# Optimization experiments

Hardware: AMD Instinct MI355X
Metric: run time of the kernel (lower is better)

The kernel has to match this reference:

```python
import jax, jax.numpy as jnp
import numpy as np

N_NODES = 100000
N_EDGES = 1600000
D_IN = 128
D_HID = 128
N_CLASS = 10
N_GRAPHS = 512
BN_EPS = 1e-5


def setup_inputs() -> dict:
    key = jax.random.key(0)
    ks = jax.random.split(key, 12)
    x = jax.random.normal(ks[0], (N_NODES, D_IN), dtype=jnp.float32)
    edge_index = jax.random.randint(ks[1], (2, N_EDGES), 0, N_NODES, dtype=jnp.int32)
    idx = jnp.sort(jax.random.randint(ks[2], (N_NODES,), 0, N_GRAPHS, dtype=jnp.int32))
    s = 1.0 / np.sqrt(D_HID)
    W1 = jax.random.uniform(ks[3], (D_IN, D_HID), minval=-s, maxval=s, dtype=jnp.float32)
    b1 = jnp.zeros((D_HID,), jnp.float32)
    W2 = jax.random.uniform(ks[4], (D_HID, D_HID), minval=-s, maxval=s, dtype=jnp.float32)
    b2 = jnp.zeros((D_HID,), jnp.float32)
    W3 = jax.random.uniform(ks[5], (D_HID, D_HID), minval=-s, maxval=s, dtype=jnp.float32)
    b3 = jnp.zeros((D_HID,), jnp.float32)
    W4 = jax.random.uniform(ks[6], (D_HID, N_CLASS), minval=-s, maxval=s, dtype=jnp.float32)
    b4 = jnp.zeros((N_CLASS,), jnp.float32)
    gamma = jnp.ones((D_HID,), jnp.float32)
    beta = jnp.zeros((D_HID,), jnp.float32)
    return {"x": x, "edge_index": edge_index, "idx": idx,
            "W1": W1, "b1": b1, "W2": W2, "b2": b2,
            "W3": W3, "b3": b3, "W4": W4, "b4": b4,
            "gamma": gamma, "beta": beta}


def _agg(h, src, dst):
    # (adj + I) @ h : sum of neighbor features plus self-loop
    return jax.ops.segment_sum(h[src], dst, num_segments=N_NODES) + h


def reference(x, edge_index, idx, W1, b1, W2, b2, W3, b3, W4, b4, gamma, beta):
    src, dst = edge_index[0], edge_index[1]
    z1 = jax.nn.relu(_agg(x, src, dst) @ W1 + b1)          # [N, H] (dropout = identity, eval)
    h = _agg(z1, src, dst) @ W2 + b2                        # [N, H]
    pooled = jax.ops.segment_sum(h, idx, num_segments=N_GRAPHS)  # [G, H] scatter-add readout
    # BatchNorm1d over graph (batch) dimension, training-mode batch stats
    mean = jnp.mean(pooled, axis=0)
    var = jnp.var(pooled, axis=0)
    out = (pooled - mean) * jax.lax.rsqrt(var + BN_EPS) * gamma + beta
    zg = jax.nn.relu(out @ W3 + b3)
    logits = zg @ W4 + b4                                   # [G, C]
    return jax.nn.log_softmax(logits, axis=1)
```

## Files before the change

kernel.cpp:

```cpp
#include <hip/hip_runtime.h>
#include <hip/hip_fp16.h>
#include <math.h>

#define NN 100000
#define NE 1600000
#define DH 128
#define NG 512
#define NC 10
#define NSEG 8
#define SEGN 12500
#define CHE 8192
#define NCH 196
#define MAXDEG 48

#define NB_HIST (NCH * NSEG)
#define NB_CNT  98
#define NB_GEMM ((NN + 63) / 64)


typedef __attribute__((ext_vector_type(8))) _Float16 f16x8;
typedef __attribute__((ext_vector_type(4))) float f32x4;
typedef __attribute__((ext_vector_type(4))) int i32x4;


__device__ __forceinline__ void upd_edge(int d, int s, int lo, int hi,
                                         int* __restrict__ counts,
                                         int* __restrict__ csr) {
    if (d >= lo && d < hi) {
        int p = atomicAdd(&counts[d], 1);
        if (p < MAXDEG) csr[d * MAXDEG + p] = s;
    }
}

__global__ __launch_bounds__(256, 8) void k_hist(
    const int* __restrict__ dst, const int* __restrict__ src,
    int* __restrict__ counts, int* __restrict__ csr,
    const int* __restrict__ gidx, int* __restrict__ cnt) {
    int b = blockIdx.x;
    int t = threadIdx.x;
    if (b < NB_HIST) {
        int seg = b & 7;
        int chunk = b >> 3;
        int lo = seg * SEGN, hi = lo + SEGN;
        int e0 = chunk * CHE;
        int e1 = e0 + CHE < NE ? e0 + CHE : NE;
        for (int e = e0 + t * 8; e < e1; e += 2048) {
            i32x4 da = __builtin_nontemporal_load((const i32x4*)(dst + e));
            i32x4 db = __builtin_nontemporal_load((const i32x4*)(dst + e + 4));
            i32x4 sa = __builtin_nontemporal_load((const i32x4*)(src + e));
            i32x4 sb = __builtin_nontemporal_load((const i32x4*)(src + e + 4));
            upd_edge(da.x, sa.x, lo, hi, counts, csr);
            upd_edge(da.y, sa.y, lo, hi, counts, csr);
            upd_edge(da.z, sa.z, lo, hi, counts, csr);
            upd_edge(da.w, sa.w, lo, hi, counts, csr);
            upd_edge(db.x, sb.x, lo, hi, counts, csr);
            upd_edge(db.y, sb.y, lo, hi, counts, csr);
            upd_edge(db.z, sb.z, lo, hi, counts, csr);
            upd_edge(db.w, sb.w, lo, hi, counts, csr);
        }
    } else {
        int cb = b - NB_HIST;
        int n0 = cb * 1024 + t * 4;
        if (n0 >= NN) return;
        int g = gidx[n0];
        int run = 1;
        for (int j = 1; j < 4; ++j) {
            int n = n0 + j;
            if (n < NN) {
                int gg = gidx[n];
                if (gg == g) {
                    run++;
                } else {
                    atomicAdd(&cnt[g], run);
                    g = gg;
                    run = 1;
                }
            }
        }
        atomicAdd(&cnt[g], run);
    }
}


__global__ __launch_bounds__(256, 4) void k_gemm(
    const float* __restrict__ A, const float* __restrict__ W,
    __half* __restrict__ out) {
    __shared__ _Float16 sWT[DH * 128];
    int gb = blockIdx.x;
    int t = threadIdx.x;
    int wv = t >> 6;
    int lane = t & 63;
    for (int i = t; i < DH * DH; i += 256) {
        int k = i >> 7, n = i & 127;
        sWT[n * 128 + (((k >> 3) ^ (n & 15)) * 8) + (k & 7)] = (_Float16)W[i];
    }
    __syncthreads();

    int m = lane & 15;
    int quad = lane >> 4;
    int node0 = gb * 64 + wv * 16;
    int nodeA = node0 + m;
    if (nodeA >= NN) nodeA = NN - 1;
    const float* arow = A + (size_t)nodeA * DH;

    f16x8 afrag[4];
#pragma unroll
    for (int kt = 0; kt < 4; ++kt) {
        int k0 = kt * 32 + quad * 8;
        f32x4 u0 = __builtin_nontemporal_load((const f32x4*)(arow + k0));
        f32x4 u1 = __builtin_nontemporal_load((const f32x4*)(arow + k0 + 4));
        afrag[kt][0] = (_Float16)u0.x; afrag[kt][1] = (_Float16)u0.y;
        afrag[kt][2] = (_Float16)u0.z; afrag[kt][3] = (_Float16)u0.w;
        afrag[kt][4] = (_Float16)u1.x; afrag[kt][5] = (_Float16)u1.y;
        afrag[kt][6] = (_Float16)u1.z; afrag[kt][7] = (_Float16)u1.w;
    }

    f32x4 acc0 = {0.f, 0.f, 0.f, 0.f};
    f32x4 acc1 = acc0, acc2 = acc0, acc3 = acc0;
    f32x4 acc4 = acc0, acc5 = acc0, acc6 = acc0, acc7 = acc0;
#pragma unroll
    for (int kt = 0; kt < 4; ++kt) {
        int kb = kt * 4 + quad;
        const _Float16* wbase = &sWT[(size_t)m * 128 + ((kb ^ m) * 8)];
        acc0 = __builtin_amdgcn_mfma_f32_16x16x32_f16(afrag[kt], *(const f16x8*)(wbase + 0 * 16 * 128), acc0, 0, 0, 0);
        acc1 = __builtin_amdgcn_mfma_f32_16x16x32_f16(afrag[kt], *(const f16x8*)(wbase + 1 * 16 * 128), acc1, 0, 0, 0);
        acc2 = __builtin_amdgcn_mfma_f32_16x16x32_f16(afrag[kt], *(const f16x8*)(wbase + 2 * 16 * 128), acc2, 0, 0, 0);
        acc3 = __builtin_amdgcn_mfma_f32_16x16x32_f16(afrag[kt], *(const f16x8*)(wbase + 3 * 16 * 128), acc3, 0, 0, 0);
        acc4 = __builtin_amdgcn_mfma_f32_16x16x32_f16(afrag[kt], *(const f16x8*)(wbase + 4 * 16 * 128), acc4, 0, 0, 0);
        acc5 = __builtin_amdgcn_mfma_f32_16x16x32_f16(afrag[kt], *(const f16x8*)(wbase + 5 * 16 * 128), acc5, 0, 0, 0);
        acc6 = __builtin_amdgcn_mfma_f32_16x16x32_f16(afrag[kt], *(const f16x8*)(wbase + 6 * 16 * 128), acc6, 0, 0, 0);
        acc7 = __builtin_amdgcn_mfma_f32_16x16x32_f16(afrag[kt], *(const f16x8*)(wbase + 7 * 16 * 128), acc7, 0, 0, 0);
    }

#pragma unroll
    for (int r = 0; r < 4; ++r) {
        int node = node0 + quad * 4 + r;
        if (node < NN) {
            uint4 o;
            *(__half2*)&o.x = __floats2half2_rn(acc0[r], acc1[r]);
            *(__half2*)&o.y = __floats2half2_rn(acc2[r], acc3[r]);
            *(__half2*)&o.z = __floats2half2_rn(acc4[r], acc5[r]);
            *(__half2*)&o.w = __floats2half2_rn(acc6[r], acc7[r]);
            ((uint4*)out)[(size_t)node * 16 + m] = o;
        }
    }
}


__device__ __forceinline__ void acc8(float* a, const uint4& v, float m) {
    float2 f;
    f = __half22float2(*(const __half2*)&v.x); a[0] = fmaf(m, f.x, a[0]); a[1] = fmaf(m, f.y, a[1]);
    f = __half22float2(*(const __half2*)&v.y); a[2] = fmaf(m, f.x, a[2]); a[3] = fmaf(m, f.y, a[3]);
    f = __half22float2(*(const __half2*)&v.z); a[4] = fmaf(m, f.x, a[4]); a[5] = fmaf(m, f.y, a[5]);
    f = __half22float2(*(const __half2*)&v.w); a[6] = fmaf(m, f.x, a[6]); a[7] = fmaf(m, f.y, a[7]);
}


__global__ __launch_bounds__(256, 4) void k_agg_h(
    const __half* __restrict__ in, const int* __restrict__ counts,
    const int* __restrict__ csr, const float* __restrict__ bias,
    __half* __restrict__ outA) {
    int t = threadIdx.x;
    int lane = t & 15;
    int node = blockIdx.x * 16 + (t >> 4);
    const uint4* in4 = (const uint4*)in;
    float a[8];
#pragma unroll
    for (int j = 0; j < 8; ++j) a[j] = 0.f;
    uint4 sv = in4[(size_t)node * 16 + lane];
    acc8(a, sv, 1.f);
    int e0 = node * MAXDEG;
    int deg = counts[node];
    deg = deg < MAXDEG ? deg : MAXDEG;
    int e1 = e0 + deg;
    int elast = e1 - 1;
    for (int e = e0; e < e1; e += 8) {
        int idx[8];
        float m[8];
#pragma unroll
        for (int i = 0; i < 8; ++i) {
            int ei = e + i;
            int ec = ei < elast ? ei : elast;
            idx[i] = csr[ec];
            m[i] = (ei < e1) ? 1.f : 0.f;
        }
        uint4 v[8];
#pragma unroll
        for (int i = 0; i < 8; ++i) v[i] = in4[(size_t)idx[i] * 16 + lane];
#pragma unroll
        for (int i = 0; i < 8; ++i) acc8(a, v[i], m[i]);
    }
    float bj[8];
#pragma unroll
    for (int j = 0; j < 8; ++j) bj[j] = bias[j * 16 + lane];
#pragma unroll
    for (int j = 0; j < 8; ++j) a[j] = fmaxf(a[j] + bj[j], 0.f);
    uint4 o;
    *(__half2*)&o.x = __floats2half2_rn(a[0], a[1]);
    *(__half2*)&o.y = __floats2half2_rn(a[2], a[3]);
    *(__half2*)&o.z = __floats2half2_rn(a[4], a[5]);
    *(__half2*)&o.w = __floats2half2_rn(a[6], a[7]);
    ((uint4*)outA)[(size_t)node * 16 + lane] = o;
}


__global__ __launch_bounds__(256, 4) void k_agg_pool_h(
    const __half* __restrict__ in, const int* __restrict__ counts,
    const int* __restrict__ csr, const int* __restrict__ gidx,
    float* __restrict__ pp8) {
    __shared__ __align__(16) float sA[16][DH];
    int t = threadIdx.x;
    int lane = t & 15;
    int p = t >> 4;
    int node0 = blockIdx.x * 16;
    int node = node0 + p;
    const uint4* in4 = (const uint4*)in;
    float a[8];
#pragma unroll
    for (int j = 0; j < 8; ++j) a[j] = 0.f;
    uint4 sv = in4[(size_t)node * 16 + lane];
    acc8(a, sv, 1.f);
    int e0 = node * MAXDEG;
    int deg = counts[node];
    deg = deg < MAXDEG ? deg : MAXDEG;
    int e1 = e0 + deg;
    int elast = e1 - 1;
    for (int e = e0; e < e1; e += 8) {
        int idx[8];
        float m[8];
#pragma unroll
        for (int i = 0; i < 8; ++i) {
            int ei = e + i;
            int ec = ei < elast ? ei : elast;
            idx[i] = csr[ec];
            m[i] = (ei < e1) ? 1.f : 0.f;
        }
        uint4 v[8];
#pragma unroll
        for (int i = 0; i < 8; ++i) v[i] = in4[(size_t)idx[i] * 16 + lane];
#pragma unroll
        for (int i = 0; i < 8; ++i) acc8(a, v[i], m[i]);
    }
    float4* row = (float4*)&sA[p][lane * 8];
    row[0] = make_float4(a[0], a[1], a[2], a[3]);
    row[1] = make_float4(a[4], a[5], a[6], a[7]);
    __syncthreads();
    if (t < DH) {
        float* pp = pp8 + (size_t)(blockIdx.x & 7) * NG * DH;
        int gprev = gidx[node0];
        float run = 0.f;
        for (int q = 0; q < 16; ++q) {
            int g = gidx[node0 + q];
            if (g != gprev) {
                atomicAdd(&pp[gprev * DH + t], run);
                run = 0.f;
                gprev = g;
            }
            run += sA[q][t];
        }
        atomicAdd(&pp[gprev * DH + t], run);
    }
}


__device__ __forceinline__ void fma4(float4& acc, float s, const float4& wv) {
    acc.x = fmaf(s, wv.x, acc.x);
    acc.y = fmaf(s, wv.y, acc.y);
    acc.z = fmaf(s, wv.z, acc.z);
    acc.w = fmaf(s, wv.w, acc.w);
}


__global__ __launch_bounds__(256, 2) void k_pool_mm(
    const float* __restrict__ pp8, const float* __restrict__ W,
    const float* __restrict__ bias, const int* __restrict__ cnt,
    float* __restrict__ pooled) {
    __shared__ __align__(16) float sW[DH * DH];
    __shared__ __align__(16) float sA[32 * DH];
    int t = threadIdx.x;
    int g0 = blockIdx.x * 32;
    {
        const float4* W4g = (const float4*)W;
        float4* sW4 = (float4*)sW;
        for (int i = t; i < DH * DH / 4; i += 256) {
            int r = i >> 5;
            int orig = ((r & 7) << 4) + (r >> 3);
            sW4[i] = W4g[orig * 32 + (i & 31)];
        }
        const float4* P4 = (const float4*)pp8;
        float4* sA4 = (float4*)sA;
        for (int i = t; i < 32 * DH / 4; i += 256) {
            float4 s;
            s.x = 0.f; s.y = 0.f; s.z = 0.f; s.w = 0.f;
#pragma unroll
            for (int c = 0; c < NSEG; ++c) {
                float4 v = P4[(size_t)c * NG * DH / 4 + (size_t)g0 * DH / 4 + i];
                s.x += v.x; s.y += v.y; s.z += v.z; s.w += v.w;
            }
            sA4[i] = s;
        }
    }
    __syncthreads();

    int c4 = t & 31;
    int n0 = (t >> 5) * 4;
    const float4* sA4 = (const float4*)sA;
    const float4* sW4 = (const float4*)sW;
    float4 acc0, acc1, acc2, acc3;
    acc0.x = acc0.y = acc0.z = acc0.w = 0.f;
    acc1 = acc0; acc2 = acc0; acc3 = acc0;

#pragma unroll 2
    for (int kc = 0; kc < DH / 4; ++kc) {
        float4 a0 = sA4[(n0 + 0) * 32 + kc];
        float4 a1 = sA4[(n0 + 1) * 32 + kc];
        float4 a2 = sA4[(n0 + 2) * 32 + kc];
        float4 a3 = sA4[(n0 + 3) * 32 + kc];
        float4 w0 = sW4[(4 * kc + 0) * 32 + c4];
        float4 w1 = sW4[(4 * kc + 1) * 32 + c4];
        float4 w2 = sW4[(4 * kc + 2) * 32 + c4];
        float4 w3 = sW4[(4 * kc + 3) * 32 + c4];
        fma4(acc0, a0.x, w0); fma4(acc0, a0.y, w1); fma4(acc0, a0.z, w2); fma4(acc0, a0.w, w3);
        fma4(acc1, a1.x, w0); fma4(acc1, a1.y, w1); fma4(acc1, a1.z, w2); fma4(acc1, a1.w, w3);
        fma4(acc2, a2.x, w0); fma4(acc2, a2.y, w1); fma4(acc2, a2.z, w2); fma4(acc2, a2.w, w3);
        fma4(acc3, a3.x, w0); fma4(acc3, a3.y, w1); fma4(acc3, a3.z, w2); fma4(acc3, a3.w, w3);
    }

    float4 b2v = ((const float4*)bias)[c4];
    float c0 = (float)cnt[g0 + n0 + 0];
    float c1 = (float)cnt[g0 + n0 + 1];
    float c2 = (float)cnt[g0 + n0 + 2];
    float c3 = (float)cnt[g0 + n0 + 3];
    fma4(acc0, c0, b2v);
    fma4(acc1, c1, b2v);
    fma4(acc2, c2, b2v);
    fma4(acc3, c3, b2v);

    float4* out4 = (float4*)pooled;
    out4[(size_t)(g0 + n0 + 0) * 32 + c4] = acc0;
    out4[(size_t)(g0 + n0 + 1) * 32 + c4] = acc1;
    out4[(size_t)(g0 + n0 + 2) * 32 + c4] = acc2;
    out4[(size_t)(g0 + n0 + 3) * 32 + c4] = acc3;
}


__global__ void k_bnstats(const float* __restrict__ pooled, float* __restrict__ mean,
                          float* __restrict__ rstd) {
    int c = blockIdx.x;
    int l = threadIdx.x;
    float s = 0.f, s2 = 0.f;
    for (int g = l; g < NG; g += 64) {
        float v = pooled[g * DH + c];
        s += v;
        s2 += v * v;
    }
#pragma unroll
    for (int off = 32; off > 0; off >>= 1) {
        s += __shfl_down(s, off, 64);
        s2 += __shfl_down(s2, off, 64);
    }
    if (l == 0) {
        float m = s * (1.f / NG);
        float var = s2 * (1.f / NG) - m * m;
        mean[c] = m;
        rstd[c] = rsqrtf(var + 1e-5f);
    }
}


__global__ __launch_bounds__(128) void k_tail(
    const float* __restrict__ pooled, const float* __restrict__ mean,
    const float* __restrict__ rstd, const float* __restrict__ gamma,
    const float* __restrict__ beta, const float* __restrict__ W3,
    const float* __restrict__ b3, const float* __restrict__ W4,
    const float* __restrict__ b4, float* __restrict__ out) {
    __shared__ __align__(16) float sW[DH * DH];
    __shared__ float sg[DH];
    __shared__ float sz[DH];
    __shared__ float slog[NC];
    __shared__ float slse;
    int g = blockIdx.x, t = threadIdx.x;
    {
        const float4* W34 = (const float4*)W3;
        float4* sW4 = (float4*)sW;
        for (int i = t; i < DH * DH / 4; i += 128) sW4[i] = W34[i];
    }
    float v = pooled[g * DH + t];
    v = (v - mean[t]) * rstd[t] * gamma[t] + beta[t];
    sg[t] = v;
    __syncthreads();
    float acc = b3[t];
#pragma unroll 4
    for (int k = 0; k < DH; ++k) acc = fmaf(sg[k], sW[k * DH + t], acc);
    sz[t] = fmaxf(acc, 0.f);
    __syncthreads();
    if (t < NC) {
        float a = b4[t];
        for (int k = 0; k < DH; ++k) a = fmaf(sz[k], W4[k * NC + t], a);
        slog[t] = a;
    }
    __syncthreads();
    if (t == 0) {
        float mx = slog[0];
        for (int j = 1; j < NC; ++j) mx = fmaxf(mx, slog[j]);
        float se = 0.f;
        for (int j = 0; j < NC; ++j) se += expf(slog[j] - mx);
        slse = mx + logf(se);
    }
    __syncthreads();
    if (t < NC) out[g * NC + t] = slog[t] - slse;
}


extern "C" void kernel_launch(void* const* d_in, const int* in_sizes, int n_in,
                              void* d_out, int out_size, void* d_ws, size_t ws_size,
                              hipStream_t stream) {
    const float* x = (const float*)d_in[0];
    const int* ei = (const int*)d_in[1];
    const int* src = ei;
    const int* dst = ei + NE;
    const int* gidx = (const int*)d_in[2];
    const float* W1 = (const float*)d_in[3];
    const float* b1 = (const float*)d_in[4];
    const float* W2 = (const float*)d_in[5];
    const float* b2 = (const float*)d_in[6];
    const float* W3 = (const float*)d_in[7];
    const float* b3 = (const float*)d_in[8];
    const float* W4 = (const float*)d_in[9];
    const float* b4 = (const float*)d_in[10];
    const float* gamma = (const float*)d_in[11];
    const float* beta = (const float*)d_in[12];
    float* out = (float*)d_out;

    char* w = (char*)d_ws;
    auto take = [&](size_t bytes) {
        char* p = w;
        w += (bytes + 255) & ~size_t(255);
        return p;
    };
    int* counts = (int*)take((size_t)NN * 4);
    int* cnt = (int*)take((size_t)NG * 4);
    float* pp8 = (float*)take((size_t)NSEG * NG * DH * 4);
    size_t zero_bytes = (size_t)((char*)(pp8 + (size_t)NSEG * NG * DH) - (char*)counts);
    int* csr = (int*)take((size_t)NN * MAXDEG * 4);
    __half* y = (__half*)take((size_t)NN * DH * 2);
    __half* z1 = (__half*)take((size_t)NN * DH * 2);
    float* pooled = (float*)take((size_t)NG * DH * 4);
    float* meanb = (float*)take(DH * 4);
    float* rstdb = (float*)take(DH * 4);

    hipMemsetAsync(counts, 0, zero_bytes, stream);

    k_hist<<<NB_HIST + NB_CNT, 256, 0, stream>>>(dst, src, counts, csr, gidx, cnt);
    k_gemm<<<NB_GEMM, 256, 0, stream>>>(x, W1, y);

    k_agg_h<<<NN / 16, 256, 0, stream>>>(y, counts, csr, b1, z1);

    k_agg_pool_h<<<NN / 16, 256, 0, stream>>>(z1, counts, csr, gidx, pp8);
    k_pool_mm<<<NG / 32, 256, 0, stream>>>(pp8, W2, b2, cnt, pooled);

    k_bnstats<<<DH, 64, 0, stream>>>(pooled, meanb, rstdb);
    k_tail<<<NG, 128, 0, stream>>>(pooled, meanb, rstdb, gamma, beta, W3, b3, W4, b4, out);
}
```

Measured before the change: 375.7 us.

## Replace segmented edge histogram with flat single-pass CSR build; raise agg occupancy

```diff
diff --git a/kernel.cpp b/kernel.cpp
--- a/kernel.cpp
+++ b/kernel.cpp
@@ -7,15 +7,11 @@
 #define DH 128
 #define NG 512
 #define NC 10
-#define NSEG 8
-#define SEGN 12500
-#define CHE 8192
-#define NCH 196
 #define MAXDEG 48
 
-#define NB_HIST (NCH * NSEG)
-#define NB_CNT  98
-#define NB_GEMM ((NN + 63) / 64)
+#define NB_HISTP ((NE + 1023) / 1024)
+#define NB_CNT   98
+#define NB_GEMM  ((NN + 63) / 64)
 
 
 typedef __attribute__((ext_vector_type(8))) _Float16 f16x8;
@@ -23,13 +19,11 @@
 typedef __attribute__((ext_vector_type(4))) int i32x4;
 
 
-__device__ __forceinline__ void upd_edge(int d, int s, int lo, int hi,
-                                         int* __restrict__ counts,
-                                         int* __restrict__ csr) {
-    if (d >= lo && d < hi) {
-        int p = atomicAdd(&counts[d], 1);
-        if (p < MAXDEG) csr[d * MAXDEG + p] = s;
-    }
+__device__ __forceinline__ void upd1(int d, int s,
+                                     int* __restrict__ counts,
+                                     int* __restrict__ csr) {
+    int p = atomicAdd(&counts[d], 1);
+    if (p < MAXDEG) csr[d * MAXDEG + p] = s;
 }
 
 __global__ __launch_bounds__(256, 8) void k_hist(
@@ -38,28 +32,18 @@
     const int* __restrict__ gidx, int* __restrict__ cnt) {
     int b = blockIdx.x;
     int t = threadIdx.x;
-    if (b < NB_HIST) {
-        int seg = b & 7;
-        int chunk = b >> 3;
-        int lo = seg * SEGN, hi = lo + SEGN;
-        int e0 = chunk * CHE;
-        int e1 = e0 + CHE < NE ? e0 + CHE : NE;
-        for (int e = e0 + t * 8; e < e1; e += 2048) {
-            i32x4 da = __builtin_nontemporal_load((const i32x4*)(dst + e));
-            i32x4 db = __builtin_nontemporal_load((const i32x4*)(dst + e + 4));
-            i32x4 sa = __builtin_nontemporal_load((const i32x4*)(src + e));
-            i32x4 sb = __builtin_nontemporal_load((const i32x4*)(src + e + 4));
-            upd_edge(da.x, sa.x, lo, hi, counts, csr);
-            upd_edge(da.y, sa.y, lo, hi, counts, csr);
-            upd_edge(da.z, sa.z, lo, hi, counts, csr);
-            upd_edge(da.w, sa.w, lo, hi, counts, csr);
-            upd_edge(db.x, sb.x, lo, hi, counts, csr);
-            upd_edge(db.y, sb.y, lo, hi, counts, csr);
-            upd_edge(db.z, sb.z, lo, hi, counts, csr);
-            upd_edge(db.w, sb.w, lo, hi, counts, csr);
+    if (b < NB_HISTP) {
+        int e = b * 1024 + t * 4;
+        if (e < NE) {
+            i32x4 d4 = __builtin_nontemporal_load((const i32x4*)(dst + e));
+            i32x4 s4 = __builtin_nontemporal_load((const i32x4*)(src + e));
+            upd1(d4.x, s4.x, counts, csr);
+            upd1(d4.y, s4.y, counts, csr);
+            upd1(d4.z, s4.z, counts, csr);
+            upd1(d4.w, s4.w, counts, csr);
         }
     } else {
-        int cb = b - NB_HIST;
+        int cb = b - NB_HISTP;
         int n0 = cb * 1024 + t * 4;
         if (n0 >= NN) return;
         int g = gidx[n0];
@@ -156,7 +140,7 @@
 }
 
 
-__global__ __launch_bounds__(256, 4) void k_agg_h(
+__global__ __launch_bounds__(256, 6) void k_agg_h(
     const __half* __restrict__ in, const int* __restrict__ counts,
     const int* __restrict__ csr, const float* __restrict__ bias,
     __half* __restrict__ outA) {
@@ -204,7 +188,7 @@
 }
 
 
-__global__ __launch_bounds__(256, 4) void k_agg_pool_h(
+__global__ __launch_bounds__(256, 6) void k_agg_pool_h(
     const __half* __restrict__ in, const int* __restrict__ counts,
     const int* __restrict__ csr, const int* __restrict__ gidx,
     float* __restrict__ pp8) {
@@ -293,7 +277,7 @@
             float4 s;
             s.x = 0.f; s.y = 0.f; s.z = 0.f; s.w = 0.f;
 #pragma unroll
-            for (int c = 0; c < NSEG; ++c) {
+            for (int c = 0; c < 8; ++c) {
                 float4 v = P4[(size_t)c * NG * DH / 4 + (size_t)g0 * DH / 4 + i];
                 s.x += v.x; s.y += v.y; s.z += v.z; s.w += v.w;
             }
@@ -440,8 +424,8 @@
     };
     int* counts = (int*)take((size_t)NN * 4);
     int* cnt = (int*)take((size_t)NG * 4);
-    float* pp8 = (float*)take((size_t)NSEG * NG * DH * 4);
-    size_t zero_bytes = (size_t)((char*)(pp8 + (size_t)NSEG * NG * DH) - (char*)counts);
+    float* pp8 = (float*)take((size_t)8 * NG * DH * 4);
+    size_t zero_bytes = (size_t)((char*)(pp8 + (size_t)8 * NG * DH) - (char*)counts);
     int* csr = (int*)take((size_t)NN * MAXDEG * 4);
     __half* y = (__half*)take((size_t)NN * DH * 2);
     __half* z1 = (__half*)take((size_t)NN * DH * 2);
@@ -451,7 +435,7 @@
 
     hipMemsetAsync(counts, 0, zero_bytes, stream);
 
-    k_hist<<<NB_HIST + NB_CNT, 256, 0, stream>>>(dst, src, counts, csr, gidx, cnt);
+    k_hist<<<NB_HISTP + NB_CNT, 256, 0, stream>>>(dst, src, counts, csr, gidx, cnt);
     k_gemm<<<NB_GEMM, 256, 0, stream>>>(x, W1, y);
 
     k_agg_h<<<NN / 16, 256, 0, stream>>>(y, counts, csr, b1, z1);
```

After: 447.1 us. 19.0% more time.
